# Kernel tuning notes

Measured on AMD Instinct MI355X. Metric: run time of the kernel, lower is better.

## Reference

```python
import jax, jax.numpy as jnp
import numpy as np

N = 2048
H = W = 128


def setup_inputs() -> dict:
    key = jax.random.key(0)
    ks = jax.random.split(key, 8)
    # Gaussians placed in front of a pinhole camera at the origin (+z forward)
    xy = jax.random.normal(ks[0], (N, 2), dtype=jnp.float32) * 1.5
    z = jax.random.uniform(ks[1], (N, 1), dtype=jnp.float32, minval=2.0, maxval=6.0)
    mean = jnp.concatenate([xy, z], axis=-1)
    qvec = jax.random.normal(ks[2], (N, 4), dtype=jnp.float32)
    # raw scales -> exp activation gives scales around 0.05
    svec_raw = jax.random.normal(ks[3], (N, 3), dtype=jnp.float32) * 0.3 - 3.0
    color_raw = jax.random.normal(ks[4], (N, 3), dtype=jnp.float32)
    alpha_raw = jax.random.normal(ks[5], (N,), dtype=jnp.float32)
    bg = jax.random.uniform(ks[6], (3,), dtype=jnp.float32)
    viewmat = jnp.eye(4, dtype=jnp.float32)
    intrins = jnp.array([120.0, 120.0, W / 2.0, H / 2.0], dtype=jnp.float32)  # fx fy cx cy
    return dict(mean=mean, qvec=qvec, svec_raw=svec_raw, color_raw=color_raw,
                alpha_raw=alpha_raw, bg=bg, viewmat=viewmat, intrins=intrins)


def _quat_to_rotmat(q):
    q = q / jnp.linalg.norm(q, axis=-1, keepdims=True)
    w, x, y, z = q[..., 0], q[..., 1], q[..., 2], q[..., 3]
    R = jnp.stack([
        1 - 2 * (y * y + z * z), 2 * (x * y - w * z), 2 * (x * z + w * y),
        2 * (x * y + w * z), 1 - 2 * (x * x + z * z), 2 * (y * z - w * x),
        2 * (x * z - w * y), 2 * (y * z + w * x), 1 - 2 * (x * x + y * y),
    ], axis=-1)
    return R.reshape(q.shape[:-1] + (3, 3))


def reference(mean, qvec, svec_raw, color_raw, alpha_raw, bg, viewmat, intrins):
    fx, fy, cx, cy = intrins[0], intrins[1], intrins[2], intrins[3]
    # activations used by GaussianSplattingRenderer (svec_act=exp, alpha/color=sigmoid)
    svec = jnp.exp(svec_raw)
    alpha = jax.nn.sigmoid(alpha_raw)
    color = jax.nn.sigmoid(color_raw)

    Rw = viewmat[:3, :3]
    tw = viewmat[:3, 3]
    p_cam = mean @ Rw.T + tw                      # (N,3)
    x, y, z = p_cam[:, 0], p_cam[:, 1], p_cam[:, 2]
    zc = jnp.maximum(z, 1e-3)

    # 3D covariance Sigma = R diag(s)^2 R^T  via  M = R diag(s),  Sigma = M M^T
    Rq = _quat_to_rotmat(qvec)                    # (N,3,3)
    M = Rq * svec[:, None, :]                     # (N,3,3)

    # perspective Jacobian (EWA splatting), composed with view rotation
    zeros = jnp.zeros_like(zc)
    J = jnp.stack([
        jnp.stack([fx / zc, zeros, -fx * x / (zc * zc)], axis=-1),
        jnp.stack([zeros, fy / zc, -fy * y / (zc * zc)], axis=-1),
    ], axis=-2)                                   # (N,2,3)
    T = jnp.einsum('nij,jk->nik', J, Rw)          # (N,2,3)
    TM = jnp.einsum('nij,njk->nik', T, M)         # (N,2,3)
    cov2d = jnp.einsum('nij,nkj->nik', TM, TM)    # (N,2,2)
    cov2d = cov2d + 0.3 * jnp.eye(2, dtype=cov2d.dtype)  # low-pass filter

    a = cov2d[:, 0, 0]; b = cov2d[:, 0, 1]; c = cov2d[:, 1, 1]
    det = a * c - b * b
    det_safe = jnp.maximum(det, 1e-8)
    conic_a = c / det_safe; conic_b = -b / det_safe; conic_c = a / det_safe

    # projected 2D means
    u = fx * x / zc + cx
    v = fy * y / zc + cy

    px = jnp.arange(W, dtype=jnp.float32) + 0.5
    py = jnp.arange(H, dtype=jnp.float32) + 0.5
    dx = px[:, None] - u[None, :]                 # (W,N)
    dy = py[:, None] - v[None, :]                 # (H,N)

    power = (-0.5 * (conic_a * dx * dx)[None, :, :]
             - 0.5 * (conic_c * dy * dy)[:, None, :]
             - conic_b[None, None, :] * dx[None, :, :] * dy[:, None, :])  # (H,W,N)
    g = jnp.exp(jnp.minimum(power, 0.0))
    valid = (z > 0.2) & (det > 0)
    alpha_pix = jnp.where(valid[None, None, :], jnp.minimum(0.99, alpha * g), 0.0)

    # front-to-back depth order, sequential alpha compositing via cumprod
    order = jnp.argsort(z)
    alpha_s = alpha_pix[:, :, order]              # (H,W,N)
    color_s = color[order]                        # (N,3)
    Tcum = jnp.cumprod(1.0 - alpha_s, axis=-1)
    Tprev = jnp.concatenate([jnp.ones_like(Tcum[..., :1]), Tcum[..., :-1]], axis=-1)
    wgt = alpha_s * Tprev                         # (H,W,N)
    img = jnp.einsum('hwn,nc->hwc', wgt, color_s) + Tcum[..., -1:] * bg
    return img
```

## Files before the change

### kernel.cpp

```cpp
#include <hip/hip_runtime.h>
#include <hip/hip_fp16.h>
#include <math.h>

#define NG 2048
#define IMG_W 128
#define IMG_H 128
#define NPIX (IMG_W * IMG_H)
#define L2E 1.4426950408889634f

struct __align__(16) PG {
    float u, v, A, B;
    float C, alpha;
    unsigned int rg;
    unsigned int b_r2;
};

__global__ __launch_bounds__(256) void prep_kernel(
    const float* __restrict__ mean, const float* __restrict__ qvec,
    const float* __restrict__ svec_raw, const float* __restrict__ color_raw,
    const float* __restrict__ alpha_raw, const float* __restrict__ viewmat,
    const float* __restrict__ intrins, PG* __restrict__ graw,
    float* __restrict__ zbuf)
{
    const int g = blockIdx.x * 256 + threadIdx.x;
    if (g >= NG) return;

    const float fx = intrins[0], fy = intrins[1], cx = intrins[2], cy = intrins[3];
    const float R00 = viewmat[0], R01 = viewmat[1], R02 = viewmat[2],  t0 = viewmat[3];
    const float R10 = viewmat[4], R11 = viewmat[5], R12 = viewmat[6],  t1 = viewmat[7];
    const float R20 = viewmat[8], R21 = viewmat[9], R22 = viewmat[10], t2 = viewmat[11];

    float mx = mean[g * 3 + 0], my = mean[g * 3 + 1], mz = mean[g * 3 + 2];
    float x = R00 * mx + R01 * my + R02 * mz + t0;
    float y = R10 * mx + R11 * my + R12 * mz + t1;
    float z = R20 * mx + R21 * my + R22 * mz + t2;
    float zc = fmaxf(z, 0.001f);

    float qw = qvec[g * 4 + 0], qx = qvec[g * 4 + 1];
    float qy = qvec[g * 4 + 2], qz = qvec[g * 4 + 3];
    float qn = rsqrtf(qw * qw + qx * qx + qy * qy + qz * qz);
    qw *= qn; qx *= qn; qy *= qn; qz *= qn;
    float Rq00 = 1.f - 2.f * (qy * qy + qz * qz), Rq01 = 2.f * (qx * qy - qw * qz), Rq02 = 2.f * (qx * qz + qw * qy);
    float Rq10 = 2.f * (qx * qy + qw * qz), Rq11 = 1.f - 2.f * (qx * qx + qz * qz), Rq12 = 2.f * (qy * qz - qw * qx);
    float Rq20 = 2.f * (qx * qz - qw * qy), Rq21 = 2.f * (qy * qz + qw * qx), Rq22 = 1.f - 2.f * (qx * qx + qy * qy);

    float s0 = expf(svec_raw[g * 3 + 0]);
    float s1 = expf(svec_raw[g * 3 + 1]);
    float s2 = expf(svec_raw[g * 3 + 2]);
    float M00 = Rq00 * s0, M01 = Rq01 * s1, M02 = Rq02 * s2;
    float M10 = Rq10 * s0, M11 = Rq11 * s1, M12 = Rq12 * s2;
    float M20 = Rq20 * s0, M21 = Rq21 * s1, M22 = Rq22 * s2;

    float iz = 1.0f / zc;
    float J00 = fx * iz, J02 = -fx * x * iz * iz;
    float J11 = fy * iz, J12 = -fy * y * iz * iz;
    float T00 = J00 * R00 + J02 * R20;
    float T01 = J00 * R01 + J02 * R21;
    float T02 = J00 * R02 + J02 * R22;
    float T10 = J11 * R10 + J12 * R20;
    float T11 = J11 * R11 + J12 * R21;
    float T12 = J11 * R12 + J12 * R22;
    float TM00 = T00 * M00 + T01 * M10 + T02 * M20;
    float TM01 = T00 * M01 + T01 * M11 + T02 * M21;
    float TM02 = T00 * M02 + T01 * M12 + T02 * M22;
    float TM10 = T10 * M00 + T11 * M10 + T12 * M20;
    float TM11 = T10 * M01 + T11 * M11 + T12 * M21;
    float TM12 = T10 * M02 + T11 * M12 + T12 * M22;
    float a = TM00 * TM00 + TM01 * TM01 + TM02 * TM02 + 0.3f;
    float b = TM00 * TM10 + TM01 * TM11 + TM02 * TM12;
    float c = TM10 * TM10 + TM11 * TM11 + TM12 * TM12 + 0.3f;
    float det = a * c - b * b;
    float det_safe = fmaxf(det, 1e-8f);
    float inv_det = 1.0f / det_safe;
    bool valid = (z > 0.2f) && (det > 0.0f);
    float alpha = 1.0f / (1.0f + expf(-alpha_raw[g]));

    float conic_a = c * inv_det;
    float conic_b = -b * inv_det;
    float conic_c = a * inv_det;

    float half_tr = 0.5f * (conic_a + conic_c);
    float half_df = 0.5f * (conic_a - conic_c);
    float lam_min = half_tr - sqrtf(half_df * half_df + conic_b * conic_b);
    float r2 = (lam_min > 1e-20f) ? (1.05f * 2.0f * 24.0f / (L2E * lam_min)) : 3.0e38f;
    if (!valid) r2 = -1.0f;

    PG pg;
    pg.u = fx * x * iz + cx;
    pg.v = fy * y * iz + cy;
    pg.A = -0.5f * L2E * conic_a;
    pg.B = -L2E * conic_b;
    pg.C = -0.5f * L2E * conic_c;
    pg.alpha = alpha;
    float cr  = 1.0f / (1.0f + expf(-color_raw[g * 3 + 0]));
    float cg  = 1.0f / (1.0f + expf(-color_raw[g * 3 + 1]));
    float cbl = 1.0f / (1.0f + expf(-color_raw[g * 3 + 2]));
    __half2 hrg = __floats2half2_rn(cr, cg);
    pg.rg = *reinterpret_cast<unsigned int*>(&hrg);
    __half2 hbr = __halves2half2(__float2half_rn(cbl), __float2half_rn(r2));
    pg.b_r2 = *reinterpret_cast<unsigned int*>(&hbr);
    graw[g] = pg;
    zbuf[g] = z;
}

__global__ __launch_bounds__(256) void rank_scatter_kernel(
    const float* __restrict__ zbuf, const PG* __restrict__ graw,
    PG* __restrict__ gsorted)
{
    const int g = (blockIdx.x * 256 + threadIdx.x) >> 6;
    const int lane = threadIdx.x & 63;
    const float zg = zbuf[g];
    const float4* z4 = (const float4*)zbuf;
    int cnt = 0;
#pragma unroll
    for (int k = 0; k < NG / 256; ++k) {
        int idx = k * 64 + lane;
        float4 zz = z4[idx];
        int h = idx * 4;
        cnt += ((zz.x < zg) || ((zz.x == zg) && (h + 0 < g))) ? 1 : 0;
        cnt += ((zz.y < zg) || ((zz.y == zg) && (h + 1 < g))) ? 1 : 0;
        cnt += ((zz.z < zg) || ((zz.z == zg) && (h + 2 < g))) ? 1 : 0;
        cnt += ((zz.w < zg) || ((zz.w == zg) && (h + 3 < g))) ? 1 : 0;
    }
#pragma unroll
    for (int off = 32; off >= 1; off >>= 1)
        cnt += __shfl_down(cnt, off);
    int rank = __shfl(cnt, 0);
    if (lane < 2) {
        ((float4*)(gsorted + rank))[lane] = ((const float4*)(graw + g))[lane];
    }
}

__device__ __forceinline__ float rlf(float x, int i) {
    return __int_as_float(__builtin_amdgcn_readlane(__float_as_int(x), i));
}
__device__ __forceinline__ unsigned rlu(float x, int i) {
    return (unsigned)__builtin_amdgcn_readlane(__float_as_int(x), i);
}

__global__ __launch_bounds__(256) void composite_tile_kernel(
    const PG* __restrict__ gsorted, const float* __restrict__ bg,
    float* __restrict__ out)
{
    __shared__ float4 part[4][64];
    const int t = threadIdx.x;
    const int wave = t >> 6;
    const int lane = t & 63;
    const int tx = blockIdx.x, ty = blockIdx.y;
    const int col = tx * 8 + (lane & 7);
    const int row = ty * 8 + (lane >> 3);

    const float x0 = tx * 8 + 0.5f, x1 = x0 + 7.0f;
    const float y0 = ty * 8 + 0.5f, y1 = y0 + 7.0f;
    const float fpx = col + 0.5f;
    const float fpy = row + 0.5f;

    float T = 1.f, Cr = 0.f, Cg = 0.f, Cb = 0.f;

    constexpr int SEG = NG / 4;
    constexpr int NCHUNK = SEG / 64;
    const float4* src = (const float4*)(gsorted + wave * SEG);
    float4 n0 = src[2 * lane + 0];
    float4 n1 = src[2 * lane + 1];

    for (int c = 0; c < NCHUNK; ++c) {
        float4 g0 = n0, g1 = n1;
        if (c + 1 < NCHUNK) {
            n0 = src[2 * ((c + 1) * 64 + lane) + 0];
            n1 = src[2 * ((c + 1) * 64 + lane) + 1];
        }

        union { float f; __half2 h; } ubr; ubr.f = g1.w;
        float r2 = __half2float(__high2half(ubr.h));
        float dxm = fmaxf(0.f, fmaxf(x0 - g0.x, g0.x - x1));
        float dym = fmaxf(0.f, fmaxf(y0 - g0.y, g0.y - y1));
        unsigned long long mask = __ballot((dxm * dxm + dym * dym) <= r2);

        while (mask) {
            int i = (int)__builtin_ctzll(mask);
            mask &= (mask - 1);
            float u  = rlf(g0.x, i), v  = rlf(g0.y, i);
            float A  = rlf(g0.z, i), B  = rlf(g0.w, i);
            float Cc = rlf(g1.x, i), al = rlf(g1.y, i);
            unsigned rgb = rlu(g1.z, i);
            unsigned brb = rlu(g1.w, i);
            union { unsigned u; __half2 h; } urg; urg.u = rgb;
            union { unsigned u; __half2 h; } ubl; ubl.u = brb;
            float cr = __half2float(__low2half(urg.h));
            float cg = __half2float(__high2half(urg.h));
            float cb = __half2float(__low2half(ubl.h));

            float dx = fpx - u;
            float adx2 = A * dx * dx;
            float bdx = B * dx;
            float dy = fpy - v;
            float p = fminf(fmaf(dy, fmaf(Cc, dy, bdx), adx2), 0.f);
            float gv = exp2f(p);
            float a = fminf(0.99f, al * gv);
            float w = a * T;
            Cr = fmaf(w, cr, Cr); Cg = fmaf(w, cg, Cg); Cb = fmaf(w, cb, Cb);
            T = fmaf(-a, T, T);
        }

        if (__all(T < 1e-6f)) break;
    }

    part[wave][lane] = make_float4(Cr, Cg, Cb, T);
    __syncthreads();

    if (wave == 0) {
        float4 p0 = part[0][lane];
        float4 p1 = part[1][lane];
        float4 p2 = part[2][lane];
        float4 p3 = part[3][lane];
        float t01 = p0.w * p1.w;
        float t012 = t01 * p2.w;
        float R = p0.x + p0.w * p1.x + t01 * p2.x + t012 * p3.x;
        float G = p0.y + p0.w * p1.y + t01 * p2.y + t012 * p3.y;
        float Bc = p0.z + p0.w * p1.z + t01 * p2.z + t012 * p3.z;
        float Tt = t012 * p3.w;
        const int pix = row * IMG_W + col;
        out[pix * 3 + 0] = R + Tt * bg[0];
        out[pix * 3 + 1] = G + Tt * bg[1];
        out[pix * 3 + 2] = Bc + Tt * bg[2];
    }
}

extern "C" void kernel_launch(void* const* d_in, const int* in_sizes, int n_in,
                              void* d_out, int out_size, void* d_ws, size_t ws_size,
                              hipStream_t stream)
{
    const float* mean      = (const float*)d_in[0];
    const float* qvec      = (const float*)d_in[1];
    const float* svec_raw  = (const float*)d_in[2];
    const float* color_raw = (const float*)d_in[3];
    const float* alpha_raw = (const float*)d_in[4];
    const float* bg        = (const float*)d_in[5];
    const float* viewmat   = (const float*)d_in[6];
    const float* intrins   = (const float*)d_in[7];
    char* ws = (char*)d_ws;
    float* out = (float*)d_out;

    PG* graw    = (PG*)ws;
    float* zbuf = (float*)(ws + NG * sizeof(PG));
    PG* gsorted = (PG*)(ws + NG * sizeof(PG) + NG * sizeof(float));

    hipLaunchKernelGGL(prep_kernel, dim3(NG / 256), dim3(256), 0, stream,
                       mean, qvec, svec_raw, color_raw, alpha_raw, viewmat,
                       intrins, graw, zbuf);
    hipLaunchKernelGGL(rank_scatter_kernel, dim3(NG * 64 / 256), dim3(256),
                       0, stream, zbuf, graw, gsorted);
    hipLaunchKernelGGL(composite_tile_kernel, dim3(16, 16), dim3(256), 0,
                       stream, gsorted, bg, out);
}
```

Baseline: 78.25 us.

## Fuse prep, sort and composite into one per-tile kernel with local culling

Result: slower. 80.87 us (+3.3%).

```diff
diff --git a/kernel.cpp b/kernel.cpp
--- a/kernel.cpp
+++ b/kernel.cpp
@@ -1,35 +1,33 @@
 #include <hip/hip_runtime.h>
-#include <hip/hip_fp16.h>
 #include <math.h>
 
 #define NG 2048
 #define IMG_W 128
 #define IMG_H 128
-#define NPIX (IMG_W * IMG_H)
 #define L2E 1.4426950408889634f
 
-struct __align__(16) PG {
-    float u, v, A, B;
-    float C, alpha;
-    unsigned int rg;
-    unsigned int b_r2;
+typedef unsigned long long u64;
+
+__device__ __forceinline__ float rlf(float x, int i) {
+    return __int_as_float(__builtin_amdgcn_readlane(__float_as_int(x), i));
+}
+
+struct PrepOut {
+    float u, v, A, B, C, al, cr, cg, cb, z, r2;
 };
 
-__global__ __launch_bounds__(256) void prep_kernel(
+template <bool COLORS>
+__device__ __forceinline__ PrepOut prep_g(
+    int g,
     const float* __restrict__ mean, const float* __restrict__ qvec,
     const float* __restrict__ svec_raw, const float* __restrict__ color_raw,
-    const float* __restrict__ alpha_raw, const float* __restrict__ viewmat,
-    const float* __restrict__ intrins, PG* __restrict__ graw,
-    float* __restrict__ zbuf)
-{
-    const int g = blockIdx.x * 256 + threadIdx.x;
-    if (g >= NG) return;
-
-    const float fx = intrins[0], fy = intrins[1], cx = intrins[2], cy = intrins[3];
-    const float R00 = viewmat[0], R01 = viewmat[1], R02 = viewmat[2],  t0 = viewmat[3];
-    const float R10 = viewmat[4], R11 = viewmat[5], R12 = viewmat[6],  t1 = viewmat[7];
-    const float R20 = viewmat[8], R21 = viewmat[9], R22 = viewmat[10], t2 = viewmat[11];
-
+    const float* __restrict__ alpha_raw,
+    float fx, float fy, float cx, float cy,
+    float R00, float R01, float R02, float t0,
+    float R10, float R11, float R12, float t1,
+    float R20, float R21, float R22, float t2)
+{
+    PrepOut o;
     float mx = mean[g * 3 + 0], my = mean[g * 3 + 1], mz = mean[g * 3 + 2];
     float x = R00 * mx + R01 * my + R02 * mz + t0;
     float y = R10 * mx + R11 * my + R12 * mz + t1;
@@ -73,7 +71,6 @@
     float det_safe = fmaxf(det, 1e-8f);
     float inv_det = 1.0f / det_safe;
     bool valid = (z > 0.2f) && (det > 0.0f);
-    float alpha = 1.0f / (1.0f + expf(-alpha_raw[g]));
 
     float conic_a = c * inv_det;
     float conic_b = -b * inv_det;
@@ -85,123 +82,147 @@
     float r2 = (lam_min > 1e-20f) ? (1.05f * 2.0f * 24.0f / (L2E * lam_min)) : 3.0e38f;
     if (!valid) r2 = -1.0f;
 
-    PG pg;
-    pg.u = fx * x * iz + cx;
-    pg.v = fy * y * iz + cy;
-    pg.A = -0.5f * L2E * conic_a;
-    pg.B = -L2E * conic_b;
-    pg.C = -0.5f * L2E * conic_c;
-    pg.alpha = alpha;
-    float cr  = 1.0f / (1.0f + expf(-color_raw[g * 3 + 0]));
-    float cg  = 1.0f / (1.0f + expf(-color_raw[g * 3 + 1]));
-    float cbl = 1.0f / (1.0f + expf(-color_raw[g * 3 + 2]));
-    __half2 hrg = __floats2half2_rn(cr, cg);
-    pg.rg = *reinterpret_cast<unsigned int*>(&hrg);
-    __half2 hbr = __halves2half2(__float2half_rn(cbl), __float2half_rn(r2));
-    pg.b_r2 = *reinterpret_cast<unsigned int*>(&hbr);
-    graw[g] = pg;
-    zbuf[g] = z;
-}
-
-__global__ __launch_bounds__(256) void rank_scatter_kernel(
-    const float* __restrict__ zbuf, const PG* __restrict__ graw,
-    PG* __restrict__ gsorted)
-{
-    const int g = (blockIdx.x * 256 + threadIdx.x) >> 6;
-    const int lane = threadIdx.x & 63;
-    const float zg = zbuf[g];
-    const float4* z4 = (const float4*)zbuf;
-    int cnt = 0;
+    o.u = fx * x * iz + cx;
+    o.v = fy * y * iz + cy;
+    o.A = -0.5f * L2E * conic_a;
+    o.B = -L2E * conic_b;
+    o.C = -0.5f * L2E * conic_c;
+    o.z = z;
+    o.r2 = r2;
+    if (COLORS) {
+        o.al = 1.0f / (1.0f + expf(-alpha_raw[g]));
+        o.cr = 1.0f / (1.0f + expf(-color_raw[g * 3 + 0]));
+        o.cg = 1.0f / (1.0f + expf(-color_raw[g * 3 + 1]));
+        o.cb = 1.0f / (1.0f + expf(-color_raw[g * 3 + 2]));
+    } else {
+        o.al = o.cr = o.cg = o.cb = 0.f;
+    }
+    return o;
+}
+
+template <int NO>
+__device__ __forceinline__ void sort_ranks(const u64* zkey,
+                                           unsigned short* ssid,
+                                           int K, int t)
+{
+    u64 myk[NO];
+    int myr[NO];
 #pragma unroll
-    for (int k = 0; k < NG / 256; ++k) {
-        int idx = k * 64 + lane;
-        float4 zz = z4[idx];
-        int h = idx * 4;
-        cnt += ((zz.x < zg) || ((zz.x == zg) && (h + 0 < g))) ? 1 : 0;
-        cnt += ((zz.y < zg) || ((zz.y == zg) && (h + 1 < g))) ? 1 : 0;
-        cnt += ((zz.z < zg) || ((zz.z == zg) && (h + 2 < g))) ? 1 : 0;
-        cnt += ((zz.w < zg) || ((zz.w == zg) && (h + 3 < g))) ? 1 : 0;
-    }
+    for (int o = 0; o < NO; ++o) {
+        int j = t + 256 * o;
+        myk[o] = (j < K) ? zkey[j] : ~0ull;
+        myr[o] = 0;
+    }
+    const ulonglong2* z2 = (const ulonglong2*)zkey;
+    const int np = (K + 1) >> 1;
+    for (int i = 0; i < np; ++i) {
+        ulonglong2 kk = z2[i];
 #pragma unroll
-    for (int off = 32; off >= 1; off >>= 1)
-        cnt += __shfl_down(cnt, off);
-    int rank = __shfl(cnt, 0);
-    if (lane < 2) {
-        ((float4*)(gsorted + rank))[lane] = ((const float4*)(graw + g))[lane];
-    }
-}
-
-__device__ __forceinline__ float rlf(float x, int i) {
-    return __int_as_float(__builtin_amdgcn_readlane(__float_as_int(x), i));
-}
-__device__ __forceinline__ unsigned rlu(float x, int i) {
-    return (unsigned)__builtin_amdgcn_readlane(__float_as_int(x), i);
-}
-
-__global__ __launch_bounds__(256) void composite_tile_kernel(
-    const PG* __restrict__ gsorted, const float* __restrict__ bg,
+        for (int o = 0; o < NO; ++o) {
+            myr[o] += (kk.x < myk[o]) ? 1 : 0;
+            myr[o] += (kk.y < myk[o]) ? 1 : 0;
+        }
+    }
+#pragma unroll
+    for (int o = 0; o < NO; ++o) {
+        int j = t + 256 * o;
+        if (j < K) ssid[myr[o]] = (unsigned short)(myk[o] & 0xFFFFu);
+    }
+}
+
+__global__ __launch_bounds__(256) void splat_kernel(
+    const float* __restrict__ mean, const float* __restrict__ qvec,
+    const float* __restrict__ svec_raw, const float* __restrict__ color_raw,
+    const float* __restrict__ alpha_raw, const float* __restrict__ bg,
+    const float* __restrict__ viewmat, const float* __restrict__ intrins,
     float* __restrict__ out)
 {
+    __shared__ __align__(16) u64 zkey[NG + 2];
+    __shared__ unsigned short ssid[NG];
     __shared__ float4 part[4][64];
+    __shared__ int scnt;
+
     const int t = threadIdx.x;
     const int wave = t >> 6;
     const int lane = t & 63;
     const int tx = blockIdx.x, ty = blockIdx.y;
-    const int col = tx * 8 + (lane & 7);
-    const int row = ty * 8 + (lane >> 3);
+
+    if (t == 0) scnt = 0;
+
+    const float fx = intrins[0], fy = intrins[1], cx = intrins[2], cy = intrins[3];
+    const float R00 = viewmat[0], R01 = viewmat[1], R02 = viewmat[2],  t0 = viewmat[3];
+    const float R10 = viewmat[4], R11 = viewmat[5], R12 = viewmat[6],  t1 = viewmat[7];
+    const float R20 = viewmat[8], R21 = viewmat[9], R22 = viewmat[10], t2 = viewmat[11];
 
     const float x0 = tx * 8 + 0.5f, x1 = x0 + 7.0f;
     const float y0 = ty * 8 + 0.5f, y1 = y0 + 7.0f;
-    const float fpx = col + 0.5f;
-    const float fpy = row + 0.5f;
-
+
+    __syncthreads();
+
+    for (int k = 0; k < 8; ++k) {
+        int g = k * 256 + t;
+        PrepOut p = prep_g<false>(g, mean, qvec, svec_raw, color_raw,
+                                  alpha_raw, fx, fy, cx, cy,
+                                  R00, R01, R02, t0, R10, R11, R12, t1,
+                                  R20, R21, R22, t2);
+        float dxm = fmaxf(0.f, fmaxf(x0 - p.u, p.u - x1));
+        float dym = fmaxf(0.f, fmaxf(y0 - p.v, p.v - y1));
+        if (dxm * dxm + dym * dym <= p.r2) {
+            int slot = atomicAdd(&scnt, 1);
+            zkey[slot] = ((u64)__float_as_uint(p.z) << 16) | (unsigned)g;
+        }
+    }
+    __syncthreads();
+    const int K = scnt;
+    if (t == 0) zkey[K] = ~0ull;
+    __syncthreads();
+
+    {
+        const int nt = (K + 255) >> 8;
+        if (nt <= 1)      sort_ranks<1>(zkey, ssid, K, t);
+        else if (nt == 2) sort_ranks<2>(zkey, ssid, K, t);
+        else if (nt == 3) sort_ranks<3>(zkey, ssid, K, t);
+        else if (nt == 4) sort_ranks<4>(zkey, ssid, K, t);
+        else              sort_ranks<8>(zkey, ssid, K, t);
+    }
+    __syncthreads();
+
+    const float fpx = tx * 8 + (lane & 7) + 0.5f;
+    const float fpy = ty * 8 + (lane >> 3) + 0.5f;
     float T = 1.f, Cr = 0.f, Cg = 0.f, Cb = 0.f;
 
-    constexpr int SEG = NG / 4;
-    constexpr int NCHUNK = SEG / 64;
-    const float4* src = (const float4*)(gsorted + wave * SEG);
-    float4 n0 = src[2 * lane + 0];
-    float4 n1 = src[2 * lane + 1];
-
-    for (int c = 0; c < NCHUNK; ++c) {
-        float4 g0 = n0, g1 = n1;
-        if (c + 1 < NCHUNK) {
-            n0 = src[2 * ((c + 1) * 64 + lane) + 0];
-            n1 = src[2 * ((c + 1) * 64 + lane) + 1];
-        }
-
-        union { float f; __half2 h; } ubr; ubr.f = g1.w;
-        float r2 = __half2float(__high2half(ubr.h));
-        float dxm = fmaxf(0.f, fmaxf(x0 - g0.x, g0.x - x1));
-        float dym = fmaxf(0.f, fmaxf(y0 - g0.y, g0.y - y1));
-        unsigned long long mask = __ballot((dxm * dxm + dym * dym) <= r2);
-
+    const int Kq = (K + 3) >> 2;
+    const int s0 = wave * Kq;
+    const int s1 = min(K, s0 + Kq);
+
+    for (int base = s0; base < s1; base += 64) {
+        const int j = base + lane;
+        const bool inr = (j < s1);
+        const int idx = inr ? (int)ssid[j] : 0;
+        PrepOut p = prep_g<true>(idx, mean, qvec, svec_raw, color_raw,
+                                 alpha_raw, fx, fy, cx, cy,
+                                 R00, R01, R02, t0, R10, R11, R12, t1,
+                                 R20, R21, R22, t2);
+        u64 mask = __ballot(inr);
         while (mask) {
-            int i = (int)__builtin_ctzll(mask);
-            mask &= (mask - 1);
-            float u  = rlf(g0.x, i), v  = rlf(g0.y, i);
-            float A  = rlf(g0.z, i), B  = rlf(g0.w, i);
-            float Cc = rlf(g1.x, i), al = rlf(g1.y, i);
-            unsigned rgb = rlu(g1.z, i);
-            unsigned brb = rlu(g1.w, i);
-            union { unsigned u; __half2 h; } urg; urg.u = rgb;
-            union { unsigned u; __half2 h; } ubl; ubl.u = brb;
-            float cr = __half2float(__low2half(urg.h));
-            float cg = __half2float(__high2half(urg.h));
-            float cb = __half2float(__low2half(ubl.h));
-
-            float dx = fpx - u;
-            float adx2 = A * dx * dx;
-            float bdx = B * dx;
-            float dy = fpy - v;
-            float p = fminf(fmaf(dy, fmaf(Cc, dy, bdx), adx2), 0.f);
-            float gv = exp2f(p);
+            const int i = (int)__builtin_ctzll(mask);
+            mask &= mask - 1;
+            float gu = rlf(p.u, i), gv_ = rlf(p.v, i);
+            float gA = rlf(p.A, i), gB = rlf(p.B, i), gC = rlf(p.C, i);
+            float al = rlf(p.al, i);
+            float cr = rlf(p.cr, i), cg = rlf(p.cg, i), cb = rlf(p.cb, i);
+
+            float dx = fpx - gu;
+            float dy = fpy - gv_;
+            float adx2 = gA * dx * dx;
+            float bdx = gB * dx;
+            float pw = fminf(fmaf(dy, fmaf(gC, dy, bdx), adx2), 0.f);
+            float gv = exp2f(pw);
             float a = fminf(0.99f, al * gv);
             float w = a * T;
             Cr = fmaf(w, cr, Cr); Cg = fmaf(w, cg, Cg); Cb = fmaf(w, cb, Cb);
             T = fmaf(-a, T, T);
         }
-
         if (__all(T < 1e-6f)) break;
     }
 
@@ -219,6 +240,8 @@
         float G = p0.y + p0.w * p1.y + t01 * p2.y + t012 * p3.y;
         float Bc = p0.z + p0.w * p1.z + t01 * p2.z + t012 * p3.z;
         float Tt = t012 * p3.w;
+        const int col = tx * 8 + (lane & 7);
+        const int row = ty * 8 + (lane >> 3);
         const int pix = row * IMG_W + col;
         out[pix * 3 + 0] = R + Tt * bg[0];
         out[pix * 3 + 1] = G + Tt * bg[1];
@@ -238,18 +261,10 @@
     const float* bg        = (const float*)d_in[5];
     const float* viewmat   = (const float*)d_in[6];
     const float* intrins   = (const float*)d_in[7];
-    char* ws = (char*)d_ws;
     float* out = (float*)d_out;
-
-    PG* graw    = (PG*)ws;
-    float* zbuf = (float*)(ws + NG * sizeof(PG));
-    PG* gsorted = (PG*)(ws + NG * sizeof(PG) + NG * sizeof(float));
-
-    hipLaunchKernelGGL(prep_kernel, dim3(NG / 256), dim3(256), 0, stream,
-                       mean, qvec, svec_raw, color_raw, alpha_raw, viewmat,
-                       intrins, graw, zbuf);
-    hipLaunchKernelGGL(rank_scatter_kernel, dim3(NG * 64 / 256), dim3(256),
-                       0, stream, zbuf, graw, gsorted);
-    hipLaunchKernelGGL(composite_tile_kernel, dim3(16, 16), dim3(256), 0,
-                       stream, gsorted, bg, out);
-}
+    (void)d_ws; (void)ws_size;
+
+    hipLaunchKernelGGL(splat_kernel, dim3(16, 16), dim3(256), 0, stream,
+                       mean, qvec, svec_raw, color_raw, alpha_raw, bg,
+                       viewmat, intrins, out);
+}
```
